# Optimization experiments

Hardware: AMD Instinct MI355X
Metric: run time of the kernel (lower is better)

## Reference

```python
import jax, jax.numpy as jnp
import numpy as np

NEG_SLOPE = 0.2


def _gat_layer(x, src, dst, n, W, a_src, a_dst, b, concat):
    """PyG-style GATConv (inference, self-loops already in src/dst).
    x: [N, Fin]; W: [Fin, H*C]; a_src/a_dst: [H, C]; b: [H*C] or [C]."""
    H, C = a_src.shape
    h = (x @ W).reshape(-1, H, C)                      # [N, H, C]
    al_s = jnp.einsum('nhc,hc->nh', h, a_src)          # [N, H]
    al_d = jnp.einsum('nhc,hc->nh', h, a_dst)          # [N, H]
    e = al_s[src] + al_d[dst]                          # [E, H]
    e = jnp.where(e >= 0, e, NEG_SLOPE * e)            # LeakyReLU(0.2)
    m = jax.ops.segment_max(e, dst, num_segments=n)    # [N, H] softmax over dst
    e = jnp.exp(e - m[dst])
    s = jax.ops.segment_sum(e, dst, num_segments=n)    # [N, H]
    alpha = e / (s[dst] + 1e-16)                       # [E, H]
    msg = h[src] * alpha[:, :, None]                   # [E, H, C]
    out = jax.ops.segment_sum(msg, dst, num_segments=n)  # [N, H, C]
    if concat:
        out = out.reshape(-1, H * C)
    else:
        out = out.mean(axis=1)
    return out + b


def _forward(x, edge_index, W1, as1, ad1, b1, W2, as2, ad2, b2, W3, as3, ad3, b3):
    n = x.shape[0]
    loops = jnp.arange(n, dtype=edge_index.dtype)
    src = jnp.concatenate([edge_index[0], loops])      # add self-loops (PyG default)
    dst = jnp.concatenate([edge_index[1], loops])
    x = _gat_layer(x, src, dst, n, W1, as1, ad1, b1, concat=True)
    x = jax.nn.elu(x)
    x = _gat_layer(x, src, dst, n, W2, as2, ad2, b2, concat=True)
    x = jax.nn.elu(x)
    x = _gat_layer(x, src, dst, n, W3, as3, ad3, b3, concat=False)
    return x


def setup_inputs() -> dict:
    key = jax.random.key(0)
    ks = jax.random.split(key, 16)
    N, E, FIN, HID, H, OUT = 50000, 320000, 256, 64, 4, 64
    sc = 0.1  # keep attention logits in a sane range
    return {
        'x': jax.random.normal(ks[0], (N, FIN), jnp.float32),
        'edge_index': jax.random.randint(ks[1], (2, E), 0, N, jnp.int32),
        'W1': jax.random.normal(ks[2], (FIN, H * HID), jnp.float32) * sc,
        'as1': jax.random.normal(ks[3], (H, HID), jnp.float32) * sc,
        'ad1': jax.random.normal(ks[4], (H, HID), jnp.float32) * sc,
        'b1': jax.random.normal(ks[5], (H * HID,), jnp.float32) * sc,
        'W2': jax.random.normal(ks[6], (H * HID, H * HID), jnp.float32) * sc,
        'as2': jax.random.normal(ks[7], (H, HID), jnp.float32) * sc,
        'ad2': jax.random.normal(ks[8], (H, HID), jnp.float32) * sc,
        'b2': jax.random.normal(ks[9], (H * HID,), jnp.float32) * sc,
        'W3': jax.random.normal(ks[10], (H * HID, OUT), jnp.float32) * sc,
        'as3': jax.random.normal(ks[11], (1, OUT), jnp.float32) * sc,
        'ad3': jax.random.normal(ks[12], (1, OUT), jnp.float32) * sc,
        'b3': jax.random.normal(ks[13], (OUT,), jnp.float32) * sc,
    }


def reference(x, edge_index, W1, as1, ad1, b1, W2, as2, ad2, b2, W3, as3, ad3, b3):
    return _forward(x, edge_index, W1, as1, ad1, b1, W2, as2, ad2, b2, W3, as3, ad3, b3)
```

## Files before the change

kernel.cpp:

```cpp
#include <hip/hip_runtime.h>


typedef __attribute__((ext_vector_type(8))) __bf16 bf16x8;
typedef __attribute__((ext_vector_type(4))) float f32x4;
typedef _Float16 f16x8 __attribute__((ext_vector_type(8)));
typedef _Float16 f16x4 __attribute__((ext_vector_type(4)));

#define NEG_SLOPE 0.2f
#define WELL 40

__device__ __forceinline__ unsigned short f2b_rne(float f) {
    unsigned int u = __float_as_uint(f);
    u += 0x7FFFu + ((u >> 16) & 1u);
    return (unsigned short)(u >> 16);
}
__device__ __forceinline__ unsigned short f2h(float f) {
    _Float16 h = (_Float16)f;
    unsigned short s;
    __builtin_memcpy(&s, &h, 2);
    return s;
}
__device__ __forceinline__ bf16x8 cvt8(const float* f) {
    unsigned short r[8];
#pragma unroll
    for (int j = 0; j < 8; j++) r[j] = f2b_rne(f[j]);
    bf16x8 v;
    __builtin_memcpy(&v, r, 16);
    return v;
}
__device__ __forceinline__ float lrelu(float e) {
    return e >= 0.f ? e : NEG_SLOPE * e;
}

__global__ __launch_bounds__(256) void k_init(const float* __restrict__ W1,
                                              const float* __restrict__ W2,
                                              const float* __restrict__ W3,
                                              unsigned short* __restrict__ W1t,
                                              unsigned short* __restrict__ W2t,
                                              unsigned short* __restrict__ W3t,
                                              int* __restrict__ cnt, int n) {
    int t = blockIdx.x * blockDim.x + threadIdx.x;
    if (t < n) cnt[t] = 0;
    const float* W;
    unsigned short* Wt;
    int Nout, idx = t;
    if (idx < 65536)        { W = W1; Wt = W1t; Nout = 256; }
    else if (idx < 131072)  { W = W2; Wt = W2t; Nout = 256; idx -= 65536; }
    else if (idx < 147456)  { W = W3; Wt = W3t; Nout = 64;  idx -= 131072; }
    else return;
    int k = idx / Nout;
    int c = idx - k * Nout;
    Wt[(size_t)c * 256 + k] = f2b_rne(W[idx]);
}

template <int NT, bool AF32, bool FILL>
__global__ __launch_bounds__(512) void k_gemm(const void* __restrict__ Av,
                                              const __bf16* __restrict__ Bt,
                                              unsigned short* __restrict__ h16,
                                              float* __restrict__ als,
                                              float* __restrict__ ald,
                                              const float* __restrict__ a_s,
                                              const float* __restrict__ a_d,
                                              int M, int H,
                                              const int* __restrict__ esrc,
                                              const int* __restrict__ edst,
                                              int* __restrict__ cnt,
                                              int* __restrict__ ell,
                                              int E, int mtiles) {
    constexpr int NN = NT * 16;
    __shared__ __align__(16) __bf16 Bs[NN][256];

    if (FILL && (int)blockIdx.x >= mtiles) {
        int t = ((int)blockIdx.x - mtiles) * (int)blockDim.x + (int)threadIdx.x;
        int stride = ((int)gridDim.x - mtiles) * (int)blockDim.x;
        for (; t < E; t += stride) {
            int d = edst[t];
            int pos = atomicAdd(&cnt[d], 1);
            if (pos < WELL) ell[(size_t)d * WELL + pos] = esrc[t];
        }
        return;
    }

    const int tid = threadIdx.x;
    const int lane = tid & 63;
    const int w = tid >> 6;
    const int i = lane & 15;
    const int quad = lane >> 4;
    const int m0 = blockIdx.x * 256;

    {
        int nl = lane >> 5;
        int p = lane & 31;
#pragma unroll
        for (int t = 0; t < NN / 16; t++) {
            int n = t * 16 + w * 2 + nl;
            int g = p ^ (n & 7);
            const __bf16* gp = Bt + (size_t)n * 256 + g * 8;
            __builtin_amdgcn_global_load_lds(
                (const __attribute__((address_space(1))) void*)gp,
                (__attribute__((address_space(3))) void*)&Bs[t * 16 + w * 2][0],
                16, 0, 0);
        }
    }

    int ra = m0 + w * 32 + i;
    int rb = ra + 16;
    if (ra >= M) ra = M - 1;
    if (rb >= M) rb = M - 1;

    f32x4 acc[2][NT] = {};
    bf16x8 afrag[2][8];

    __syncthreads();

    if (AF32) {
        const float* pa = (const float*)Av + (size_t)ra * 256;
        const float* pb = (const float*)Av + (size_t)rb * 256;
        float tmp[2][4][8];
#pragma unroll
        for (int k4 = 0; k4 < 4; k4++) {
            int koff = k4 * 32 + quad * 8;
            *(float4*)&tmp[0][k4][0] = *(const float4*)(pa + koff);
            *(float4*)&tmp[0][k4][4] = *(const float4*)(pa + koff + 4);
            *(float4*)&tmp[1][k4][0] = *(const float4*)(pb + koff);
            *(float4*)&tmp[1][k4][4] = *(const float4*)(pb + koff + 4);
        }
#pragma unroll
        for (int k4 = 0; k4 < 4; k4++) {
            afrag[0][k4] = cvt8(tmp[0][k4]);
            afrag[1][k4] = cvt8(tmp[1][k4]);
        }
#pragma unroll
        for (int k4 = 0; k4 < 4; k4++) {
            int koff = (4 + k4) * 32 + quad * 8;
            *(float4*)&tmp[0][k4][0] = *(const float4*)(pa + koff);
            *(float4*)&tmp[0][k4][4] = *(const float4*)(pa + koff + 4);
            *(float4*)&tmp[1][k4][0] = *(const float4*)(pb + koff);
            *(float4*)&tmp[1][k4][4] = *(const float4*)(pb + koff + 4);
        }
#pragma unroll
        for (int kc = 0; kc < 4; kc++) {
            const int c = kc * 4 + quad;
#pragma unroll
            for (int nt = 0; nt < NT; nt++) {
                const int n = nt * 16 + i;
                const int p = c ^ (n & 7);
                bf16x8 bfv = *(const bf16x8*)&Bs[n][p * 8];
                acc[0][nt] = __builtin_amdgcn_mfma_f32_16x16x32_bf16(
                    afrag[0][kc], bfv, acc[0][nt], 0, 0, 0);
                acc[1][nt] = __builtin_amdgcn_mfma_f32_16x16x32_bf16(
                    afrag[1][kc], bfv, acc[1][nt], 0, 0, 0);
            }
        }
#pragma unroll
        for (int k4 = 0; k4 < 4; k4++) {
            afrag[0][4 + k4] = cvt8(tmp[0][k4]);
            afrag[1][4 + k4] = cvt8(tmp[1][k4]);
        }
#pragma unroll
        for (int kc = 4; kc < 8; kc++) {
            const int c = kc * 4 + quad;
#pragma unroll
            for (int nt = 0; nt < NT; nt++) {
                const int n = nt * 16 + i;
                const int p = c ^ (n & 7);
                bf16x8 bfv = *(const bf16x8*)&Bs[n][p * 8];
                acc[0][nt] = __builtin_amdgcn_mfma_f32_16x16x32_bf16(
                    afrag[0][kc], bfv, acc[0][nt], 0, 0, 0);
                acc[1][nt] = __builtin_amdgcn_mfma_f32_16x16x32_bf16(
                    afrag[1][kc], bfv, acc[1][nt], 0, 0, 0);
            }
        }
    } else {
        const __bf16* pa = (const __bf16*)Av + (size_t)ra * 256;
        const __bf16* pb = (const __bf16*)Av + (size_t)rb * 256;
#pragma unroll
        for (int kc = 0; kc < 8; kc++) {
            int koff = kc * 32 + quad * 8;
            afrag[0][kc] = *(const bf16x8*)(pa + koff);
            afrag[1][kc] = *(const bf16x8*)(pb + koff);
        }
#pragma unroll
        for (int kc = 0; kc < 8; kc++) {
            const int c = kc * 4 + quad;
#pragma unroll
            for (int nt = 0; nt < NT; nt++) {
                const int n = nt * 16 + i;
                const int p = c ^ (n & 7);
                bf16x8 bfv = *(const bf16x8*)&Bs[n][p * 8];
                acc[0][nt] = __builtin_amdgcn_mfma_f32_16x16x32_bf16(
                    afrag[0][kc], bfv, acc[0][nt], 0, 0, 0);
                acc[1][nt] = __builtin_amdgcn_mfma_f32_16x16x32_bf16(
                    afrag[1][kc], bfv, acc[1][nt], 0, 0, 0);
            }
        }
    }

    float asv[NT], adv[NT];
#pragma unroll
    for (int nt = 0; nt < NT; nt++) {
        asv[nt] = a_s[(nt / 4) * 64 + (nt & 3) * 16 + i];
        adv[nt] = a_d[(nt / 4) * 64 + (nt & 3) * 16 + i];
    }

#pragma unroll
    for (int mt = 0; mt < 2; mt++) {
#pragma unroll
        for (int r = 0; r < 4; r++) {
            int row = m0 + w * 32 + mt * 16 + quad * 4 + r;
            bool ok = row < M;
#pragma unroll
            for (int nt = 0; nt < NT; nt++) {
                if (ok) h16[(size_t)row * NN + nt * 16 + i] = f2h(acc[mt][nt][r]);
            }
#pragma unroll
            for (int g = 0; g < (NT + 3) / 4; g++) {
                float ps = 0.f, pd = 0.f;
#pragma unroll
                for (int j = 0; j < 4 && g * 4 + j < NT; j++) {
                    float v = acc[mt][g * 4 + j][r];
                    ps += v * asv[g * 4 + j];
                    pd += v * adv[g * 4 + j];
                }
#pragma unroll
                for (int off = 1; off <= 8; off <<= 1) {
                    ps += __shfl_xor(ps, off, 64);
                    pd += __shfl_xor(pd, off, 64);
                }
                if (ok && i == 0) {
                    als[(size_t)row * H + g] = ps;
                    ald[(size_t)row * H + g] = pd;
                }
            }
        }
    }
}

__global__ __launch_bounds__(256) void k_agg4(const unsigned short* __restrict__ h16,
                                              const float* __restrict__ als,
                                              const float* __restrict__ ald,
                                              const int* __restrict__ cnt,
                                              const int* __restrict__ ell,
                                              const float* __restrict__ bias,
                                              unsigned short* __restrict__ xout,
                                              int n) {
    int gw = (blockIdx.x * blockDim.x + threadIdx.x) >> 6;
    int lane = threadIdx.x & 63;
    int wid = gw * 2 + (lane >> 5);
    if (wid >= n) return;
    int l = lane & 31;
    int head = l >> 3;
    int ch = l * 8;
    int base = lane & 32;

    int deg = min(cnt[wid], WELL);
    const int* row = ell + (size_t)wid * WELL;
    int myid = (l < deg) ? row[l] : 0;

    float aldv = ald[wid * 4 + head];
    float p = __expf(fminf(lrelu(als[wid * 4 + head] + aldv), 60.f));
    float ssum = p;
    float a[8];
    {
        f16x8 h0 = *(const f16x8*)&h16[(size_t)wid * 256 + ch];
#pragma unroll
        for (int j = 0; j < 8; j++) a[j] = p * (float)h0[j];
    }

    int jmax = min(deg, 32);
    int dm1 = deg - 1;
    for (int j = 0; j < jmax; j += 4) {
        int s0 = __shfl(myid, base + min(j, dm1));
        int s1 = __shfl(myid, base + min(j + 1, dm1));
        int s2 = __shfl(myid, base + min(j + 2, dm1));
        int s3 = __shfl(myid, base + min(j + 3, dm1));
        float e0 = als[s0 * 4 + head];
        float e1 = als[s1 * 4 + head];
        float e2 = als[s2 * 4 + head];
        float e3 = als[s3 * 4 + head];
        f16x8 v0 = *(const f16x8*)&h16[(size_t)s0 * 256 + ch];
        f16x8 v1 = *(const f16x8*)&h16[(size_t)s1 * 256 + ch];
        f16x8 v2 = *(const f16x8*)&h16[(size_t)s2 * 256 + ch];
        f16x8 v3 = *(const f16x8*)&h16[(size_t)s3 * 256 + ch];
        float p0 = __expf(fminf(lrelu(e0 + aldv), 60.f));
        float p1 = (j + 1 < deg) ? __expf(fminf(lrelu(e1 + aldv), 60.f)) : 0.f;
        float p2 = (j + 2 < deg) ? __expf(fminf(lrelu(e2 + aldv), 60.f)) : 0.f;
        float p3 = (j + 3 < deg) ? __expf(fminf(lrelu(e3 + aldv), 60.f)) : 0.f;
        ssum += (p0 + p1) + (p2 + p3);
#pragma unroll
        for (int k = 0; k < 8; k++) {
            a[k] += (p0 * (float)v0[k] + p1 * (float)v1[k]) +
                    (p2 * (float)v2[k] + p3 * (float)v3[k]);
        }
    }
    for (int j = 32; j < deg; ++j) {
        int s0 = row[j];
        float p0 = __expf(fminf(lrelu(als[s0 * 4 + head] + aldv), 60.f));
        f16x8 v0 = *(const f16x8*)&h16[(size_t)s0 * 256 + ch];
        ssum += p0;
#pragma unroll
        for (int k = 0; k < 8; k++) a[k] += p0 * (float)v0[k];
    }

    float inv = 1.f / (ssum + 1e-16f);
    float bb[8];
    *(float4*)&bb[0] = *(const float4*)&bias[ch];
    *(float4*)&bb[4] = *(const float4*)&bias[ch + 4];
    unsigned short o[8];
#pragma unroll
    for (int k = 0; k < 8; k++) {
        float r = a[k] * inv + bb[k];
        r = r > 0.f ? r : expm1f(r);
        o[k] = f2b_rne(r);
    }
    *(int4*)&xout[(size_t)wid * 256 + ch] = *(const int4*)&o[0];
}

__global__ __launch_bounds__(256) void k_agg1(const unsigned short* __restrict__ h16,
                                              const float* __restrict__ als,
                                              const float* __restrict__ ald,
                                              const int* __restrict__ cnt,
                                              const int* __restrict__ ell,
                                              const float* __restrict__ bias,
                                              float* __restrict__ out, int n) {
    int gw = (blockIdx.x * blockDim.x + threadIdx.x) >> 6;
    int lane = threadIdx.x & 63;
    int wid = gw * 8 + (lane >> 3);
    if (wid >= n) return;
    int l = lane & 7;
    int ch = l * 8;
    int base = lane & 56;

    int deg = min(cnt[wid], WELL);
    const int* row = ell + (size_t)wid * WELL;
    int myid = (l < deg) ? row[l] : 0;

    float aldv = ald[wid];
    float p = __expf(fminf(lrelu(als[wid] + aldv), 60.f));
    float ssum = p;
    float a[8];
    {
        f16x8 hv = *(const f16x8*)&h16[(size_t)wid * 64 + ch];
#pragma unroll
        for (int k = 0; k < 8; k++) a[k] = p * (float)hv[k];
    }

    int dm1 = deg - 1;
    for (int j = 0; j < deg; j += 4) {
        int i0 = min(j, dm1), i1 = min(j + 1, dm1);
        int i2 = min(j + 2, dm1), i3 = min(j + 3, dm1);
        int s0, s1, s2, s3;
        if (j < 8) {
            s0 = __shfl(myid, base + i0);
            s1 = __shfl(myid, base + i1);
            s2 = __shfl(myid, base + i2);
            s3 = __shfl(myid, base + i3);
        } else {
            s0 = row[i0]; s1 = row[i1]; s2 = row[i2]; s3 = row[i3];
        }
        float e0 = als[s0], e1 = als[s1], e2 = als[s2], e3 = als[s3];
        f16x8 v0 = *(const f16x8*)&h16[(size_t)s0 * 64 + ch];
        f16x8 v1 = *(const f16x8*)&h16[(size_t)s1 * 64 + ch];
        f16x8 v2 = *(const f16x8*)&h16[(size_t)s2 * 64 + ch];
        f16x8 v3 = *(const f16x8*)&h16[(size_t)s3 * 64 + ch];
        float p0 = __expf(fminf(lrelu(e0 + aldv), 60.f));
        float p1 = (j + 1 < deg) ? __expf(fminf(lrelu(e1 + aldv), 60.f)) : 0.f;
        float p2 = (j + 2 < deg) ? __expf(fminf(lrelu(e2 + aldv), 60.f)) : 0.f;
        float p3 = (j + 3 < deg) ? __expf(fminf(lrelu(e3 + aldv), 60.f)) : 0.f;
        ssum += (p0 + p1) + (p2 + p3);
#pragma unroll
        for (int k = 0; k < 8; k++)
            a[k] += (p0 * (float)v0[k] + p1 * (float)v1[k]) +
                    (p2 * (float)v2[k] + p3 * (float)v3[k]);
    }

    float inv = 1.f / (ssum + 1e-16f);
    float bb[8];
    *(float4*)&bb[0] = *(const float4*)&bias[ch];
    *(float4*)&bb[4] = *(const float4*)&bias[ch + 4];
    float r[8];
#pragma unroll
    for (int k = 0; k < 8; k++) r[k] = a[k] * inv + bb[k];
    *(float4*)&out[(size_t)wid * 64 + ch] = *(const float4*)&r[0];
    *(float4*)&out[(size_t)wid * 64 + ch + 4] = *(const float4*)&r[4];
}

extern "C" void kernel_launch(void* const* d_in, const int* in_sizes, int n_in,
                              void* d_out, int out_size, void* d_ws, size_t ws_size,
                              hipStream_t stream) {
    const float* x   = (const float*)d_in[0];
    const int*   ei  = (const int*)d_in[1];
    const float* W1  = (const float*)d_in[2];
    const float* as1 = (const float*)d_in[3];
    const float* ad1 = (const float*)d_in[4];
    const float* b1  = (const float*)d_in[5];
    const float* W2  = (const float*)d_in[6];
    const float* as2 = (const float*)d_in[7];
    const float* ad2 = (const float*)d_in[8];
    const float* b2  = (const float*)d_in[9];
    const float* W3  = (const float*)d_in[10];
    const float* as3 = (const float*)d_in[11];
    const float* ad3 = (const float*)d_in[12];
    const float* b3  = (const float*)d_in[13];

    const int N = in_sizes[0] / 256;
    const int E = in_sizes[1] / 2;

    size_t off = 0;
    auto alloc = [&](size_t bytes) -> void* {
        void* p = (char*)d_ws + off;
        off += (bytes + 255) & ~(size_t)255;
        return p;
    };
    unsigned short* xb  = (unsigned short*)alloc((size_t)N * 256 * 2);
    unsigned short* W1t = (unsigned short*)alloc((size_t)256 * 256 * 2);
    unsigned short* W2t = (unsigned short*)alloc((size_t)256 * 256 * 2);
    unsigned short* W3t = (unsigned short*)alloc((size_t)64 * 256 * 2);
    unsigned short* h16 = (unsigned short*)alloc((size_t)N * 256 * 2);
    float* als = (float*)alloc((size_t)N * 4 * 4);
    float* ald = (float*)alloc((size_t)N * 4 * 4);
    int* cnt   = (int*)alloc((size_t)N * 4);
    int* ell   = (int*)alloc((size_t)N * WELL * 4);

    const int T = 256;
    const int agg4_blocks = (N + 7) / 8;
    const int agg1_blocks = (N + 31) / 32;
    const int mtiles = (N + 255) / 256;

    k_init<<<dim3(576), T, 0, stream>>>(W1, W2, W3, W1t, W2t, W3t, cnt, N);

    k_gemm<16, true, true><<<dim3(mtiles + 60), 512, 0, stream>>>(
        x, (const __bf16*)W1t, h16, als, ald, as1, ad1, N, 4,
        ei, ei + E, cnt, ell, E, mtiles);
    k_agg4<<<dim3(agg4_blocks), T, 0, stream>>>(h16, als, ald, cnt, ell, b1, xb, N);

    k_gemm<16, false, false><<<dim3(mtiles), 512, 0, stream>>>(
        xb, (const __bf16*)W2t, h16, als, ald, as2, ad2, N, 4,
        nullptr, nullptr, nullptr, nullptr, 0, mtiles);
    k_agg4<<<dim3(agg4_blocks), T, 0, stream>>>(h16, als, ald, cnt, ell, b2, xb, N);

    k_gemm<4, false, false><<<dim3(mtiles), 512, 0, stream>>>(
        xb, (const __bf16*)W3t, h16, als, ald, as3, ad3, N, 1,
        nullptr, nullptr, nullptr, nullptr, 0, mtiles);
    k_agg1<<<dim3(agg1_blocks), T, 0, stream>>>(h16, als, ald, cnt, ell, b3,
                                                (float*)d_out, N);
}
```

Measured before the change: 251.0 us.

## Split GEMM tiles into 128-row by 128-column blocks for higher occupancy

The GEMM kernel now gives each block 128 rows instead of 256, and one wave computes 16 rows instead of 32. The 256-wide layers are split across two column blocks, each staging only 128 columns of B in shared memory. Launch bounds now request 4 blocks per CU, and the grid is 2x or 4x larger. This aims to raise occupancy and spread work over more CUs, which matters because the old grid of about 196 blocks underfilled the GPU. In exchange, each block re-reads the A rows (once per column block) and loads B more often, so per-block data reuse is lower.

```diff
diff --git a/kernel.cpp b/kernel.cpp
--- a/kernel.cpp
+++ b/kernel.cpp
@@ -54,7 +54,7 @@
 }
 
 template <int NT, bool AF32, bool FILL>
-__global__ __launch_bounds__(512) void k_gemm(const void* __restrict__ Av,
+__global__ __launch_bounds__(512, 4) void k_gemm(const void* __restrict__ Av,
                                               const __bf16* __restrict__ Bt,
                                               unsigned short* __restrict__ h16,
                                               float* __restrict__ als,
@@ -66,13 +66,14 @@
                                               const int* __restrict__ edst,
                                               int* __restrict__ cnt,
                                               int* __restrict__ ell,
-                                              int E, int mtiles) {
+                                              int E, int mtiles, int gblocks,
+                                              int nn_tot) {
     constexpr int NN = NT * 16;
     __shared__ __align__(16) __bf16 Bs[NN][256];
 
-    if (FILL && (int)blockIdx.x >= mtiles) {
-        int t = ((int)blockIdx.x - mtiles) * (int)blockDim.x + (int)threadIdx.x;
-        int stride = ((int)gridDim.x - mtiles) * (int)blockDim.x;
+    if (FILL && (int)blockIdx.x >= gblocks) {
+        int t = ((int)blockIdx.x - gblocks) * (int)blockDim.x + (int)threadIdx.x;
+        int stride = ((int)gridDim.x - gblocks) * (int)blockDim.x;
         for (; t < E; t += stride) {
             int d = edst[t];
             int pos = atomicAdd(&cnt[d], 1);
@@ -86,57 +87,49 @@
     const int w = tid >> 6;
     const int i = lane & 15;
     const int quad = lane >> 4;
-    const int m0 = blockIdx.x * 256;
+    const int mtile = (int)blockIdx.x % mtiles;
+    const int col0 = ((int)blockIdx.x / mtiles) * NN;
+    const int m0 = mtile * 128;
 
     {
         int nl = lane >> 5;
         int p = lane & 31;
 #pragma unroll
         for (int t = 0; t < NN / 16; t++) {
-            int n = t * 16 + w * 2 + nl;
-            int g = p ^ (n & 7);
-            const __bf16* gp = Bt + (size_t)n * 256 + g * 8;
+            int n = t * 16 + w * 2;
+            int g = p ^ ((n + nl) & 7);
+            const __bf16* gp = Bt + (size_t)(col0 + n + nl) * 256 + g * 8;
             __builtin_amdgcn_global_load_lds(
                 (const __attribute__((address_space(1))) void*)gp,
-                (__attribute__((address_space(3))) void*)&Bs[t * 16 + w * 2][0],
+                (__attribute__((address_space(3))) void*)&Bs[n][0],
                 16, 0, 0);
         }
     }
 
-    int ra = m0 + w * 32 + i;
-    int rb = ra + 16;
+    int ra = m0 + w * 16 + i;
     if (ra >= M) ra = M - 1;
-    if (rb >= M) rb = M - 1;
-
-    f32x4 acc[2][NT] = {};
-    bf16x8 afrag[2][8];
+
+    f32x4 acc[NT] = {};
+    bf16x8 afrag[8];
 
     __syncthreads();
 
     if (AF32) {
         const float* pa = (const float*)Av + (size_t)ra * 256;
-        const float* pb = (const float*)Av + (size_t)rb * 256;
-        float tmp[2][4][8];
+        float tmp[4][8];
 #pragma unroll
         for (int k4 = 0; k4 < 4; k4++) {
             int koff = k4 * 32 + quad * 8;
-            *(float4*)&tmp[0][k4][0] = *(const float4*)(pa + koff);
-            *(float4*)&tmp[0][k4][4] = *(const float4*)(pa + koff + 4);
-            *(float4*)&tmp[1][k4][0] = *(const float4*)(pb + koff);
-            *(float4*)&tmp[1][k4][4] = *(const float4*)(pb + koff + 4);
-        }
-#pragma unroll
-        for (int k4 = 0; k4 < 4; k4++) {
-            afrag[0][k4] = cvt8(tmp[0][k4]);
-            afrag[1][k4] = cvt8(tmp[1][k4]);
-        }
+            *(float4*)&tmp[k4][0] = *(const float4*)(pa + koff);
+            *(float4*)&tmp[k4][4] = *(const float4*)(pa + koff + 4);
+        }
+#pragma unroll
+        for (int k4 = 0; k4 < 4; k4++) afrag[k4] = cvt8(tmp[k4]);
 #pragma unroll
         for (int k4 = 0; k4 < 4; k4++) {
             int koff = (4 + k4) * 32 + quad * 8;
-            *(float4*)&tmp[0][k4][0] = *(const float4*)(pa + koff);
-            *(float4*)&tmp[0][k4][4] = *(const float4*)(pa + koff + 4);
-            *(float4*)&tmp[1][k4][0] = *(const float4*)(pb + koff);
-            *(float4*)&tmp[1][k4][4] = *(const float4*)(pb + koff + 4);
+            *(float4*)&tmp[k4][0] = *(const float4*)(pa + koff);
+            *(float4*)&tmp[k4][4] = *(const float4*)(pa + koff + 4);
         }
 #pragma unroll
         for (int kc = 0; kc < 4; kc++) {
@@ -146,17 +139,12 @@
                 const int n = nt * 16 + i;
                 const int p = c ^ (n & 7);
                 bf16x8 bfv = *(const bf16x8*)&Bs[n][p * 8];
-                acc[0][nt] = __builtin_amdgcn_mfma_f32_16x16x32_bf16(
-                    afrag[0][kc], bfv, acc[0][nt], 0, 0, 0);
-                acc[1][nt] = __builtin_amdgcn_mfma_f32_16x16x32_bf16(
-                    afrag[1][kc], bfv, acc[1][nt], 0, 0, 0);
-            }
-        }
-#pragma unroll
-        for (int k4 = 0; k4 < 4; k4++) {
-            afrag[0][4 + k4] = cvt8(tmp[0][k4]);
-            afrag[1][4 + k4] = cvt8(tmp[1][k4]);
-        }
+                acc[nt] = __builtin_amdgcn_mfma_f32_16x16x32_bf16(
+                    afrag[kc], bfv, acc[nt], 0, 0, 0);
+            }
+        }
+#pragma unroll
+        for (int k4 = 0; k4 < 4; k4++) afrag[4 + k4] = cvt8(tmp[k4]);
 #pragma unroll
         for (int kc = 4; kc < 8; kc++) {
             const int c = kc * 4 + quad;
@@ -165,20 +153,16 @@
                 const int n = nt * 16 + i;
                 const int p = c ^ (n & 7);
                 bf16x8 bfv = *(const bf16x8*)&Bs[n][p * 8];
-                acc[0][nt] = __builtin_amdgcn_mfma_f32_16x16x32_bf16(
-                    afrag[0][kc], bfv, acc[0][nt], 0, 0, 0);
-                acc[1][nt] = __builtin_amdgcn_mfma_f32_16x16x32_bf16(
-                    afrag[1][kc], bfv, acc[1][nt], 0, 0, 0);
+                acc[nt] = __builtin_amdgcn_mfma_f32_16x16x32_bf16(
+                    afrag[kc], bfv, acc[nt], 0, 0, 0);
             }
         }
     } else {
         const __bf16* pa = (const __bf16*)Av + (size_t)ra * 256;
-        const __bf16* pb = (const __bf16*)Av + (size_t)rb * 256;
 #pragma unroll
         for (int kc = 0; kc < 8; kc++) {
             int koff = kc * 32 + quad * 8;
-            afrag[0][kc] = *(const bf16x8*)(pa + koff);
-            afrag[1][kc] = *(const bf16x8*)(pb + koff);
+            afrag[kc] = *(const bf16x8*)(pa + koff);
         }
 #pragma unroll
         for (int kc = 0; kc < 8; kc++) {
@@ -188,10 +172,8 @@
                 const int n = nt * 16 + i;
                 const int p = c ^ (n & 7);
                 bf16x8 bfv = *(const bf16x8*)&Bs[n][p * 8];
-                acc[0][nt] = __builtin_amdgcn_mfma_f32_16x16x32_bf16(
-                    afrag[0][kc], bfv, acc[0][nt], 0, 0, 0);
-                acc[1][nt] = __builtin_amdgcn_mfma_f32_16x16x32_bf16(
-                    afrag[1][kc], bfv, acc[1][nt], 0, 0, 0);
+                acc[nt] = __builtin_amdgcn_mfma_f32_16x16x32_bf16(
+                    afrag[kc], bfv, acc[nt], 0, 0, 0);
             }
         }
     }
@@ -199,38 +181,36 @@
     float asv[NT], adv[NT];
 #pragma unroll
     for (int nt = 0; nt < NT; nt++) {
-        asv[nt] = a_s[(nt / 4) * 64 + (nt & 3) * 16 + i];
-        adv[nt] = a_d[(nt / 4) * 64 + (nt & 3) * 16 + i];
-    }
-
-#pragma unroll
-    for (int mt = 0; mt < 2; mt++) {
-#pragma unroll
-        for (int r = 0; r < 4; r++) {
-            int row = m0 + w * 32 + mt * 16 + quad * 4 + r;
-            bool ok = row < M;
-#pragma unroll
-            for (int nt = 0; nt < NT; nt++) {
-                if (ok) h16[(size_t)row * NN + nt * 16 + i] = f2h(acc[mt][nt][r]);
-            }
-#pragma unroll
-            for (int g = 0; g < (NT + 3) / 4; g++) {
-                float ps = 0.f, pd = 0.f;
-#pragma unroll
-                for (int j = 0; j < 4 && g * 4 + j < NT; j++) {
-                    float v = acc[mt][g * 4 + j][r];
-                    ps += v * asv[g * 4 + j];
-                    pd += v * adv[g * 4 + j];
-                }
-#pragma unroll
-                for (int off = 1; off <= 8; off <<= 1) {
-                    ps += __shfl_xor(ps, off, 64);
-                    pd += __shfl_xor(pd, off, 64);
-                }
-                if (ok && i == 0) {
-                    als[(size_t)row * H + g] = ps;
-                    ald[(size_t)row * H + g] = pd;
-                }
+        asv[nt] = a_s[col0 + (nt >> 2) * 64 + (nt & 3) * 16 + i];
+        adv[nt] = a_d[col0 + (nt >> 2) * 64 + (nt & 3) * 16 + i];
+    }
+
+#pragma unroll
+    for (int r = 0; r < 4; r++) {
+        int row = m0 + w * 16 + quad * 4 + r;
+        bool ok = row < M;
+#pragma unroll
+        for (int nt = 0; nt < NT; nt++) {
+            if (ok) h16[(size_t)row * nn_tot + col0 + nt * 16 + i] =
+                        f2h(acc[nt][r]);
+        }
+#pragma unroll
+        for (int g = 0; g < (NT + 3) / 4; g++) {
+            float ps = 0.f, pd = 0.f;
+#pragma unroll
+            for (int j = 0; j < 4 && g * 4 + j < NT; j++) {
+                float v = acc[g * 4 + j][r];
+                ps += v * asv[g * 4 + j];
+                pd += v * adv[g * 4 + j];
+            }
+#pragma unroll
+            for (int off = 1; off <= 8; off <<= 1) {
+                ps += __shfl_xor(ps, off, 64);
+                pd += __shfl_xor(pd, off, 64);
+            }
+            if (ok && i == 0) {
+                als[(size_t)row * H + (col0 >> 6) + g] = ps;
+                ald[(size_t)row * H + (col0 >> 6) + g] = pd;
             }
         }
     }
@@ -425,23 +405,23 @@
     const int T = 256;
     const int agg4_blocks = (N + 7) / 8;
     const int agg1_blocks = (N + 31) / 32;
-    const int mtiles = (N + 255) / 256;
+    const int mtiles = (N + 127) / 128;
 
     k_init<<<dim3(576), T, 0, stream>>>(W1, W2, W3, W1t, W2t, W3t, cnt, N);
 
-    k_gemm<16, true, true><<<dim3(mtiles + 60), 512, 0, stream>>>(
+    k_gemm<8, true, true><<<dim3(2 * mtiles + 60), 512, 0, stream>>>(
         x, (const __bf16*)W1t, h16, als, ald, as1, ad1, N, 4,
-        ei, ei + E, cnt, ell, E, mtiles);
+        ei, ei + E, cnt, ell, E, mtiles, 2 * mtiles, 256);
     k_agg4<<<dim3(agg4_blocks), T, 0, stream>>>(h16, als, ald, cnt, ell, b1, xb, N);
 
-    k_gemm<16, false, false><<<dim3(mtiles), 512, 0, stream>>>(
+    k_gemm<8, false, false><<<dim3(2 * mtiles), 512, 0, stream>>>(
         xb, (const __bf16*)W2t, h16, als, ald, as2, ad2, N, 4,
-        nullptr, nullptr, nullptr, nullptr, 0, mtiles);
+        nullptr, nullptr, nullptr, nullptr, 0, mtiles, 2 * mtiles, 256);
     k_agg4<<<dim3(agg4_blocks), T, 0, stream>>>(h16, als, ald, cnt, ell, b2, xb, N);
 
     k_gemm<4, false, false><<<dim3(mtiles), 512, 0, stream>>>(
         xb, (const __bf16*)W3t, h16, als, ald, as3, ad3, N, 1,
-        nullptr, nullptr, nullptr, nullptr, 0, mtiles);
+        nullptr, nullptr, nullptr, nullptr, 0, mtiles, mtiles, 64);
     k_agg1<<<dim3(agg1_blocks), T, 0, stream>>>(h16, als, ald, cnt, ell, b3,
                                                 (float*)d_out, N);
 }
```

New measurement: 262.6 us. 4.6% more time.

## Read GEMM B fragments directly from global memory and shrink blocks to 256 threads

Applied to the files above, without the earlier changes.

The GEMM kernel no longer stages the transposed weight matrix into LDS. Each MFMA B fragment is now loaded straight from global memory, relying on L1/L2 caching, and the LDS barrier is removed. Blocks shrink to 256 threads covering 128 rows, with launch bounds set for 4 blocks per CU, so the grid and the number of fill blocks are doubled. The aim is to drop the per-block LDS fill and sync cost and allow more blocks to reside per CU, at the cost of many redundant uncoalesced global reads of B.

```diff
diff --git a/kernel.cpp b/kernel.cpp
--- a/kernel.cpp
+++ b/kernel.cpp
@@ -54,7 +54,7 @@
 }
 
 template <int NT, bool AF32, bool FILL>
-__global__ __launch_bounds__(512) void k_gemm(const void* __restrict__ Av,
+__global__ __launch_bounds__(256, 4) void k_gemm(const void* __restrict__ Av,
                                               const __bf16* __restrict__ Bt,
                                               unsigned short* __restrict__ h16,
                                               float* __restrict__ als,
@@ -68,7 +68,6 @@
                                               int* __restrict__ ell,
                                               int E, int mtiles) {
     constexpr int NN = NT * 16;
-    __shared__ __align__(16) __bf16 Bs[NN][256];
 
     if (FILL && (int)blockIdx.x >= mtiles) {
         int t = ((int)blockIdx.x - mtiles) * (int)blockDim.x + (int)threadIdx.x;
@@ -86,22 +85,7 @@
     const int w = tid >> 6;
     const int i = lane & 15;
     const int quad = lane >> 4;
-    const int m0 = blockIdx.x * 256;
-
-    {
-        int nl = lane >> 5;
-        int p = lane & 31;
-#pragma unroll
-        for (int t = 0; t < NN / 16; t++) {
-            int n = t * 16 + w * 2 + nl;
-            int g = p ^ (n & 7);
-            const __bf16* gp = Bt + (size_t)n * 256 + g * 8;
-            __builtin_amdgcn_global_load_lds(
-                (const __attribute__((address_space(1))) void*)gp,
-                (__attribute__((address_space(3))) void*)&Bs[t * 16 + w * 2][0],
-                16, 0, 0);
-        }
-    }
+    const int m0 = blockIdx.x * 128;
 
     int ra = m0 + w * 32 + i;
     int rb = ra + 16;
@@ -110,8 +94,6 @@
 
     f32x4 acc[2][NT] = {};
     bf16x8 afrag[2][8];
-
-    __syncthreads();
 
     if (AF32) {
         const float* pa = (const float*)Av + (size_t)ra * 256;
@@ -143,9 +125,7 @@
             const int c = kc * 4 + quad;
 #pragma unroll
             for (int nt = 0; nt < NT; nt++) {
-                const int n = nt * 16 + i;
-                const int p = c ^ (n & 7);
-                bf16x8 bfv = *(const bf16x8*)&Bs[n][p * 8];
+                bf16x8 bfv = *(const bf16x8*)(Bt + (size_t)(nt * 16 + i) * 256 + c * 8);
                 acc[0][nt] = __builtin_amdgcn_mfma_f32_16x16x32_bf16(
                     afrag[0][kc], bfv, acc[0][nt], 0, 0, 0);
                 acc[1][nt] = __builtin_amdgcn_mfma_f32_16x16x32_bf16(
@@ -162,9 +142,7 @@
             const int c = kc * 4 + quad;
 #pragma unroll
             for (int nt = 0; nt < NT; nt++) {
-                const int n = nt * 16 + i;
-                const int p = c ^ (n & 7);
-                bf16x8 bfv = *(const bf16x8*)&Bs[n][p * 8];
+                bf16x8 bfv = *(const bf16x8*)(Bt + (size_t)(nt * 16 + i) * 256 + c * 8);
                 acc[0][nt] = __builtin_amdgcn_mfma_f32_16x16x32_bf16(
                     afrag[0][kc], bfv, acc[0][nt], 0, 0, 0);
                 acc[1][nt] = __builtin_amdgcn_mfma_f32_16x16x32_bf16(
@@ -185,9 +163,7 @@
             const int c = kc * 4 + quad;
 #pragma unroll
             for (int nt = 0; nt < NT; nt++) {
-                const int n = nt * 16 + i;
-                const int p = c ^ (n & 7);
-                bf16x8 bfv = *(const bf16x8*)&Bs[n][p * 8];
+                bf16x8 bfv = *(const bf16x8*)(Bt + (size_t)(nt * 16 + i) * 256 + c * 8);
                 acc[0][nt] = __builtin_amdgcn_mfma_f32_16x16x32_bf16(
                     afrag[0][kc], bfv, acc[0][nt], 0, 0, 0);
                 acc[1][nt] = __builtin_amdgcn_mfma_f32_16x16x32_bf16(
@@ -425,21 +401,21 @@
     const int T = 256;
     const int agg4_blocks = (N + 7) / 8;
     const int agg1_blocks = (N + 31) / 32;
-    const int mtiles = (N + 255) / 256;
+    const int mtiles = (N + 127) / 128;
 
     k_init<<<dim3(576), T, 0, stream>>>(W1, W2, W3, W1t, W2t, W3t, cnt, N);
 
-    k_gemm<16, true, true><<<dim3(mtiles + 60), 512, 0, stream>>>(
+    k_gemm<16, true, true><<<dim3(mtiles + 120), T, 0, stream>>>(
         x, (const __bf16*)W1t, h16, als, ald, as1, ad1, N, 4,
         ei, ei + E, cnt, ell, E, mtiles);
     k_agg4<<<dim3(agg4_blocks), T, 0, stream>>>(h16, als, ald, cnt, ell, b1, xb, N);
 
-    k_gemm<16, false, false><<<dim3(mtiles), 512, 0, stream>>>(
+    k_gemm<16, false, false><<<dim3(mtiles), T, 0, stream>>>(
         xb, (const __bf16*)W2t, h16, als, ald, as2, ad2, N, 4,
         nullptr, nullptr, nullptr, nullptr, 0, mtiles);
     k_agg4<<<dim3(agg4_blocks), T, 0, stream>>>(h16, als, ald, cnt, ell, b2, xb, N);
 
-    k_gemm<4, false, false><<<dim3(mtiles), 512, 0, stream>>>(
+    k_gemm<4, false, false><<<dim3(mtiles), T, 0, stream>>>(
         xb, (const __bf16*)W3t, h16, als, ald, as3, ad3, N, 1,
         nullptr, nullptr, nullptr, nullptr, 0, mtiles);
     k_agg1<<<dim3(agg1_blocks), T, 0, stream>>>(h16, als, ald, cnt, ell, b3,
```

New measurement: 482.3 us. 1.92x slower.
